# Kernel optimization log

Measured on AMD Instinct MI355X. Metric: run time of the kernel, lower is better.

Reference implementation:

```python
import jax, jax.numpy as jnp
import numpy as np

K_MASK = -2.3819763e+38
B, T, D, N, K, H = 2, 4096, 2048, 8, 1, 256


def apply_rope(inputs, positions, head_dim):
    # inputs: [B, T, n, H], positions: [B, T]
    fraction = 2.0 * jnp.arange(0, head_dim // 2, dtype=jnp.float32) / head_dim
    timescale = 10000.0 ** fraction  # [H/2]
    sinusoid_inp = positions[..., None].astype(jnp.float32) / timescale  # [B,T,H/2]
    sinusoid_inp = sinusoid_inp[..., None, :]  # [B,T,1,H/2]
    sin, cos = jnp.sin(sinusoid_inp), jnp.cos(sinusoid_inp)
    first_half, second_half = jnp.split(inputs, 2, axis=-1)
    first_part = first_half * cos - second_half * sin
    second_part = second_half * cos + first_half * sin
    return jnp.concatenate([first_part, second_part], axis=-1).astype(inputs.dtype)


def setup_inputs() -> dict:
    key = jax.random.key(0)
    kx, kq, kkv, ko = jax.random.split(key, 4)
    x = jax.random.normal(kx, (B, T, D), dtype=jnp.float32)
    segment_pos = jnp.broadcast_to(jnp.arange(T, dtype=jnp.int32), (B, T))
    attn_mask = jnp.broadcast_to(
        jnp.tril(jnp.ones((T, T), dtype=bool)), (B, T, T))  # causal
    q_w = jax.random.normal(kq, (N, D, H), dtype=jnp.float32) * 0.02
    kv_w = jax.random.normal(kkv, (2, K, D, H), dtype=jnp.float32) * 0.02
    out_w = jax.random.normal(ko, (N, H, D), dtype=jnp.float32) * 0.02
    return {"x": x, "segment_pos": segment_pos, "attn_mask": attn_mask,
            "q_w": q_w, "kv_w": kv_w, "out_w": out_w}


def reference(x, segment_pos, attn_mask, q_w, kv_w, out_w):
    # Projections (GQA branch: num_kv_heads != num_heads)
    query_proj = jnp.einsum('btd,ndh->btnh', x, q_w)          # [B,T,N,H]
    kv_proj = jnp.einsum('bsd,ckdh->cbskh', x, kv_w)          # [2,B,T,K,H]
    key_proj, value_proj = kv_proj[0], kv_proj[1]

    query_proj = apply_rope(query_proj, segment_pos, head_dim=H)
    query_scaled = query_proj * H ** (-0.5)
    key_proj = apply_rope(key_proj, segment_pos, head_dim=H)

    # Repeat KV heads for GQA (num_kv_heads == 1 -> N heads)
    value_proj = jnp.repeat(value_proj, N, axis=-2)           # [B,S,N,H]
    key_proj = jnp.repeat(key_proj, N, axis=-2)               # [B,S,N,H]

    logits = jnp.einsum('btnh,bsnh->btns', query_scaled, key_proj)
    padded_logits = jnp.where(attn_mask[:, :, None, :], logits, K_MASK)
    probs = jax.nn.softmax(padded_logits, axis=-1).astype(key_proj.dtype)
    encoded = jnp.einsum('btns,bsnh->btnh', probs, value_proj)
    attn_output = jnp.einsum('btnh,nhd->btd', encoded, out_w)
    return attn_output
```

## Files before the change

kernel.cpp:

```cpp
#include <hip/hip_runtime.h>

#define T_SEQ 4096
#define D_MODEL 2048
#define N_HEADS 8
#define HDIM 256

typedef unsigned int uint32;
typedef unsigned short u16;
typedef __attribute__((ext_vector_type(8))) short short8;
typedef __attribute__((ext_vector_type(4))) float f32x4;

__device__ __forceinline__ float bf2f(u16 v) {
  return __uint_as_float(((uint32)v) << 16);
}
__device__ __forceinline__ u16 f2bf(float f) {
  uint32 u = __float_as_uint(f);
  u += 0x7fffu + ((u >> 16) & 1u);
  return (u16)(u >> 16);
}
__device__ __forceinline__ uint2 pack4(const f32x4 v) {
  uint2 r;
  r.x = (uint32)f2bf(v[0]) | ((uint32)f2bf(v[1]) << 16);
  r.y = (uint32)f2bf(v[2]) | ((uint32)f2bf(v[3]) << 16);
  return r;
}
__device__ __forceinline__ void gload16(const u16* g, u16* l) {
  __builtin_amdgcn_global_load_lds(
      (const __attribute__((address_space(1))) unsigned int*)g,
      (__attribute__((address_space(3))) unsigned int*)l, 16, 0, 0);
}

__global__ __launch_bounds__(256) void convert_x(const float* __restrict__ x,
                                                 u16* __restrict__ xb) {
  const int idx = blockIdx.x * 256 + threadIdx.x;
  float4 v = *(const float4*)(x + (size_t)idx * 4);
  uint2 pk;
  pk.x = (uint32)f2bf(v.x) | ((uint32)f2bf(v.y) << 16);
  pk.y = (uint32)f2bf(v.z) | ((uint32)f2bf(v.w) << 16);
  *(uint2*)(xb + (size_t)idx * 4) = pk;
}

__global__ __launch_bounds__(256) void prep_weights(
    const float* __restrict__ qw, const float* __restrict__ kvw,
    const float* __restrict__ ow, u16* __restrict__ Wt, u16* __restrict__ Owt) {
  __shared__ float Ts[64][65];
  const int t = threadIdx.x;
  const int tx = blockIdx.x, ty = blockIdx.y, z = blockIdx.z;
  const float* src;
  int srcStride;
  u16* dst;
  if (z == 0) {
    const int c0 = tx * 64;
    const float* base = (c0 < 2048)
                            ? qw + (size_t)(c0 >> 8) * D_MODEL * HDIM
                            : kvw + (size_t)((c0 - 2048) >> 8) * D_MODEL * HDIM;
    src = base + (c0 & 255);
    srcStride = HDIM;
    dst = Wt + (size_t)c0 * D_MODEL;
  } else {
    if (tx >= 32) return;
    src = ow + tx * 64;
    srcStride = D_MODEL;
    dst = Owt + (size_t)tx * 64 * D_MODEL;
  }
  const int d0 = ty * 64;
  const int r = t >> 4, c4 = (t & 15) * 4;
#pragma unroll
  for (int i = 0; i < 4; ++i) {
    float4 v = *(const float4*)(src + (size_t)(d0 + r + i * 16) * srcStride + c4);
    *(float4*)&Ts[r + i * 16][c4] = v;
  }
  __syncthreads();
#pragma unroll
  for (int i = 0; i < 4; ++i) {
    const int crow = r + i * 16;
    uint2 pk;
    pk.x = (uint32)f2bf(Ts[c4 + 0][crow]) | ((uint32)f2bf(Ts[c4 + 1][crow]) << 16);
    pk.y = (uint32)f2bf(Ts[c4 + 2][crow]) | ((uint32)f2bf(Ts[c4 + 3][crow]) << 16);
    *(uint2*)(dst + (size_t)crow * D_MODEL + d0 + c4) = pk;
  }
}

__global__ __launch_bounds__(256) void gemm_qkv_mfma(
    const u16* __restrict__ xb, const u16* __restrict__ Wt,
    u16* __restrict__ Qb, u16* __restrict__ Kb, u16* __restrict__ Vt) {
  __shared__ u16 Asm[128][32];
  __shared__ u16 Bsm[128][32];
  const int t = threadIdx.x;
  const int w = t >> 6, l = t & 63, quad = l >> 4, lq = l & 15;
  const int wm = w & 1, wn = w >> 1;
  const int col0 = blockIdx.x * 128, row0 = blockIdx.y * 128;
  const u16* ga0 = xb + (size_t)(row0 + (t >> 2)) * D_MODEL + (t & 3) * 8;
  const u16* ga1 = ga0 + (size_t)64 * D_MODEL;
  const u16* gb0 = Wt + (size_t)(col0 + (t >> 2)) * D_MODEL + (t & 3) * 8;
  const u16* gb1 = gb0 + (size_t)64 * D_MODEL;
  u16* lA0 = &Asm[0][0] + t * 8;
  u16* lA1 = lA0 + 2048;
  u16* lB0 = &Bsm[0][0] + t * 8;
  u16* lB1 = lB0 + 2048;
  f32x4 acc[4][4];
#pragma unroll
  for (int i = 0; i < 4; ++i)
#pragma unroll
    for (int j = 0; j < 4; ++j) acc[i][j] = (f32x4){0.f, 0.f, 0.f, 0.f};
  for (int k0 = 0; k0 < D_MODEL; k0 += 32) {
    gload16(ga0 + k0, lA0);
    gload16(ga1 + k0, lA1);
    gload16(gb0 + k0, lB0);
    gload16(gb1 + k0, lB1);
    __syncthreads();
    short8 af[4], bf[4];
#pragma unroll
    for (int i = 0; i < 4; ++i)
      af[i] = *(const short8*)&Asm[wm * 64 + i * 16 + lq][quad * 8];
#pragma unroll
    for (int j = 0; j < 4; ++j)
      bf[j] = *(const short8*)&Bsm[wn * 64 + j * 16 + lq][quad * 8];
#pragma unroll
    for (int i = 0; i < 4; ++i)
#pragma unroll
      for (int j = 0; j < 4; ++j)
        acc[i][j] =
            __builtin_amdgcn_mfma_f32_16x16x32_bf16(af[i], bf[j], acc[i][j], 0, 0, 0);
    __syncthreads();
  }
  const int b = row0 >> 12, sbase = row0 & 4095;
#pragma unroll
  for (int i = 0; i < 4; ++i) {
    const int rowloc = wm * 64 + i * 16 + quad * 4;
#pragma unroll
    for (int j = 0; j < 4; ++j) {
      const int col = col0 + wn * 64 + j * 16 + lq;
      if (col < 2048) {
#pragma unroll
        for (int r = 0; r < 4; ++r)
          Qb[(size_t)(row0 + rowloc + r) * 2048 + col] = f2bf(acc[i][j][r]);
      } else if (col < 2304) {
#pragma unroll
        for (int r = 0; r < 4; ++r)
          Kb[(size_t)(row0 + rowloc + r) * HDIM + (col - 2048)] =
              f2bf(acc[i][j][r]);
      } else {
        *(uint2*)(Vt + ((size_t)b * HDIM + col - 2304) * T_SEQ + sbase + rowloc) =
            pack4(acc[i][j]);
      }
    }
  }
}

__global__ __launch_bounds__(256) void rope_kernel(u16* __restrict__ Qb,
                                                   u16* __restrict__ Kb,
                                                   const int* __restrict__ segpos) {
  const int bt = blockIdx.x;
  const int tid = threadIdx.x;
  const float fpos = (float)segpos[bt];
  const float k_ln = 9.210340371976184f / 128.0f;
  for (int p = tid; p < 1024; p += 256) {
    const int n = p >> 7, i = p & 127;
    const size_t base = (size_t)bt * (N_HEADS * HDIM) + (size_t)n * HDIM;
    const float th = fpos * expf(-(float)i * k_ln);
    float s, c;
    sincosf(th, &s, &c);
    const float f1 = bf2f(Qb[base + i]);
    const float f2 = bf2f(Qb[base + i + 128]);
    Qb[base + i] = f2bf((f1 * c - f2 * s) * 0.0625f);
    Qb[base + i + 128] = f2bf((f2 * c + f1 * s) * 0.0625f);
  }
  if (tid < 128) {
    const int i = tid;
    const size_t base = (size_t)bt * HDIM;
    const float th = fpos * expf(-(float)i * k_ln);
    float s, c;
    sincosf(th, &s, &c);
    const float f1 = bf2f(Kb[base + i]);
    const float f2 = bf2f(Kb[base + i + 128]);
    Kb[base + i] = f2bf(f1 * c - f2 * s);
    Kb[base + i + 128] = f2bf(f2 * c + f1 * s);
  }
}

__global__ __launch_bounds__(256) void attn_mfma(const u16* __restrict__ Qb,
                                                 const u16* __restrict__ Kb,
                                                 const u16* __restrict__ Vt,
                                                 u16* __restrict__ Eb) {
  __shared__ u16 Ks[32][264];
  __shared__ u16 Vs[256][40];
  __shared__ u16 Ps[4][16][40];
  const int t = threadIdx.x;
  const int w = t >> 6, l = t & 63;
  const int quad = l >> 4, lq = l & 15;
  const int bid = blockIdx.x;
  const int n = blockIdx.y, b = blockIdx.z;
  const u16* kgbase = Kb + (size_t)b * T_SEQ * HDIM;
  const u16* vgbase = Vt + (size_t)b * HDIM * T_SEQ;

#pragma unroll 1
  for (int ti = 0; ti < 2; ++ti) {
    const int qt = ti ? bid : 63 - bid;
    const int q0 = qt * 64;
    const int wrow0 = q0 + w * 16;

    short8 qf[8];
    {
      const u16* qbase = Qb +
          (((size_t)b * T_SEQ + wrow0 + lq) * N_HEADS + n) * HDIM + quad * 8;
#pragma unroll
      for (int c = 0; c < 8; ++c) qf[c] = *(const short8*)(qbase + c * 32);
    }
    f32x4 O[16];
#pragma unroll
    for (int i = 0; i < 16; ++i) O[i] = (f32x4){0.f, 0.f, 0.f, 0.f};
    float m_i[4] = {-1e30f, -1e30f, -1e30f, -1e30f};
    float l_i[4] = {0.f, 0.f, 0.f, 0.f};

    const int nst = 2 * qt + 2;
    for (int st = 0; st < nst; ++st) {
      const int s0 = st * 32;
      __syncthreads();
#pragma unroll
      for (int p = 0; p < 4; ++p) {
        const int chunk = p * 256 + t;
        const int row = chunk >> 5, col = chunk & 31;
        *(uint4*)&Ks[row][col * 8] =
            *(const uint4*)(kgbase + (size_t)(s0 + row) * HDIM + col * 8);
      }
#pragma unroll
      for (int p = 0; p < 4; ++p) {
        const int chunk = p * 256 + t;
        const int row = chunk >> 2, c4 = chunk & 3;
        *(uint4*)&Vs[row][c4 * 8] =
            *(const uint4*)(vgbase + (size_t)row * T_SEQ + s0 + c4 * 8);
      }
      __syncthreads();
      if (s0 <= wrow0 + 15) {
        f32x4 sa0 = (f32x4){0.f, 0.f, 0.f, 0.f};
        f32x4 sa1 = (f32x4){0.f, 0.f, 0.f, 0.f};
#pragma unroll
        for (int c = 0; c < 8; ++c) {
          short8 k0 = *(const short8*)&Ks[lq][c * 32 + quad * 8];
          short8 k1 = *(const short8*)&Ks[16 + lq][c * 32 + quad * 8];
          sa0 = __builtin_amdgcn_mfma_f32_16x16x32_bf16(qf[c], k0, sa0, 0, 0, 0);
          sa1 = __builtin_amdgcn_mfma_f32_16x16x32_bf16(qf[c], k1, sa1, 0, 0, 0);
        }
        if (s0 + 31 > wrow0) {
#pragma unroll
          for (int r = 0; r < 4; ++r) {
            const int rw = wrow0 + quad * 4 + r;
            if (s0 + lq > rw) sa0[r] = -1e30f;
            if (s0 + 16 + lq > rw) sa1[r] = -1e30f;
          }
        }
        float al[4];
#pragma unroll
        for (int r = 0; r < 4; ++r) {
          float mx = fmaxf(sa0[r], sa1[r]);
          mx = fmaxf(mx, __shfl_xor(mx, 1));
          mx = fmaxf(mx, __shfl_xor(mx, 2));
          mx = fmaxf(mx, __shfl_xor(mx, 4));
          mx = fmaxf(mx, __shfl_xor(mx, 8));
          const float mnew = fmaxf(m_i[r], mx);
          const float a = __expf(m_i[r] - mnew);
          const float p0 = __expf(sa0[r] - mnew);
          const float p1 = __expf(sa1[r] - mnew);
          float rs = p0 + p1;
          rs += __shfl_xor(rs, 1);
          rs += __shfl_xor(rs, 2);
          rs += __shfl_xor(rs, 4);
          rs += __shfl_xor(rs, 8);
          l_i[r] = l_i[r] * a + rs;
          m_i[r] = mnew;
          al[r] = a;
          Ps[w][quad * 4 + r][lq] = f2bf(p0);
          Ps[w][quad * 4 + r][16 + lq] = f2bf(p1);
        }
#pragma unroll
        for (int ntl = 0; ntl < 16; ++ntl) {
          O[ntl][0] *= al[0];
          O[ntl][1] *= al[1];
          O[ntl][2] *= al[2];
          O[ntl][3] *= al[3];
        }
        __asm__ volatile("s_waitcnt lgkmcnt(0)" ::: "memory");
        short8 pf = *(const short8*)&Ps[w][lq][quad * 8];
#pragma unroll
        for (int ntl = 0; ntl < 16; ++ntl) {
          short8 vf = *(const short8*)&Vs[ntl * 16 + lq][quad * 8];
          O[ntl] = __builtin_amdgcn_mfma_f32_16x16x32_bf16(pf, vf, O[ntl], 0, 0, 0);
        }
      }
    }
    float inv[4];
#pragma unroll
    for (int r = 0; r < 4; ++r) inv[r] = 1.0f / l_i[r];
    u16* ebase =
        Eb + (((size_t)b * T_SEQ + wrow0 + quad * 4) * N_HEADS + n) * HDIM + lq;
#pragma unroll
    for (int ntl = 0; ntl < 16; ++ntl)
#pragma unroll
      for (int r = 0; r < 4; ++r)
        ebase[(size_t)r * (N_HEADS * HDIM) + ntl * 16] = f2bf(O[ntl][r] * inv[r]);
  }
}

__global__ __launch_bounds__(256) void gemm_out_mfma(const u16* __restrict__ E,
                                                     const u16* __restrict__ Owt,
                                                     float* __restrict__ out) {
  __shared__ u16 Asm[128][32];
  __shared__ u16 Bsm[128][32];
  const int t = threadIdx.x;
  const int w = t >> 6, l = t & 63, quad = l >> 4, lq = l & 15;
  const int wm = w & 1, wn = w >> 1;
  const int col0 = blockIdx.x * 128, row0 = blockIdx.y * 128;
  const u16* ga0 = E + (size_t)(row0 + (t >> 2)) * D_MODEL + (t & 3) * 8;
  const u16* ga1 = ga0 + (size_t)64 * D_MODEL;
  const u16* gb0 = Owt + (size_t)(col0 + (t >> 2)) * D_MODEL + (t & 3) * 8;
  const u16* gb1 = gb0 + (size_t)64 * D_MODEL;
  u16* lA0 = &Asm[0][0] + t * 8;
  u16* lA1 = lA0 + 2048;
  u16* lB0 = &Bsm[0][0] + t * 8;
  u16* lB1 = lB0 + 2048;
  f32x4 acc[4][4];
#pragma unroll
  for (int i = 0; i < 4; ++i)
#pragma unroll
    for (int j = 0; j < 4; ++j) acc[i][j] = (f32x4){0.f, 0.f, 0.f, 0.f};
  for (int k0 = 0; k0 < D_MODEL; k0 += 32) {
    gload16(ga0 + k0, lA0);
    gload16(ga1 + k0, lA1);
    gload16(gb0 + k0, lB0);
    gload16(gb1 + k0, lB1);
    __syncthreads();
    short8 af[4], bf[4];
#pragma unroll
    for (int i = 0; i < 4; ++i)
      af[i] = *(const short8*)&Asm[wm * 64 + i * 16 + lq][quad * 8];
#pragma unroll
    for (int j = 0; j < 4; ++j)
      bf[j] = *(const short8*)&Bsm[wn * 64 + j * 16 + lq][quad * 8];
#pragma unroll
    for (int i = 0; i < 4; ++i)
#pragma unroll
      for (int j = 0; j < 4; ++j)
        acc[i][j] =
            __builtin_amdgcn_mfma_f32_16x16x32_bf16(af[i], bf[j], acc[i][j], 0, 0, 0);
    __syncthreads();
  }
#pragma unroll
  for (int i = 0; i < 4; ++i) {
    const int row = row0 + wm * 64 + i * 16 + quad * 4;
#pragma unroll
    for (int j = 0; j < 4; ++j) {
      const int col = col0 + wn * 64 + j * 16 + lq;
#pragma unroll
      for (int r = 0; r < 4; ++r)
        out[(size_t)(row + r) * D_MODEL + col] = acc[i][j][r];
    }
  }
}

extern "C" void kernel_launch(void* const* d_in, const int* in_sizes, int n_in,
                              void* d_out, int out_size, void* d_ws,
                              size_t ws_size, hipStream_t stream) {
  const float* x = (const float*)d_in[0];
  const int* segpos = (const int*)d_in[1];
  const float* qw = (const float*)d_in[3];
  const float* kvw = (const float*)d_in[4];
  const float* ow = (const float*)d_in[5];
  float* out = (float*)d_out;

  char* ws = (char*)d_ws;
  u16* Qb = (u16*)ws;
  u16* Kb = (u16*)(ws + (size_t)33554432);
  u16* Vt = (u16*)(ws + (size_t)37748736);
  u16* xb = (u16*)(ws + (size_t)41943040);
  u16* Eb = xb;
  u16* Wt = (u16*)(ws + (size_t)75497472);
  u16* Owt = (u16*)(ws + (size_t)85983232);

  hipLaunchKernelGGL(convert_x, dim3(16384), dim3(256), 0, stream, x, xb);
  hipLaunchKernelGGL(prep_weights, dim3(40, 32, 2), dim3(256), 0, stream, qw,
                     kvw, ow, Wt, Owt);
  hipLaunchKernelGGL(gemm_qkv_mfma, dim3(20, 64), dim3(256), 0, stream, xb, Wt,
                     Qb, Kb, Vt);
  hipLaunchKernelGGL(rope_kernel, dim3(8192), dim3(256), 0, stream, Qb, Kb,
                     segpos);
  hipLaunchKernelGGL(attn_mfma, dim3(32, N_HEADS, 2), dim3(256), 0, stream, Qb,
                     Kb, Vt, Eb);
  hipLaunchKernelGGL(gemm_out_mfma, dim3(16, 64), dim3(256), 0, stream, Eb, Owt,
                     out);
}
```

Measured before the change: 814.8 us.

## Read V fragments directly from global, defer row-sum reduction, skip unchanged rescale

Drops the shared-memory staging of V and loads each V fragment for the PV MFMA straight from global memory (relying on L2/L1 reuse across waves), which frees LDS and lets the launch bounds request three blocks per CU. The per-tile row-sum shuffle reduction is replaced by a per-lane partial sum, reduced once at the end. The O rescale is skipped when no row max increased in the wave. Ps padding is changed. The risk is higher global load latency and redundant V traffic in the inner loop, since each of the four waves now fetches the same V tile itself.

After: 1.156 ms. 1.42x slower.

```diff
diff --git a/kernel.cpp b/kernel.cpp
--- a/kernel.cpp
+++ b/kernel.cpp
@@ -179,13 +179,12 @@
   }
 }
 
-__global__ __launch_bounds__(256) void attn_mfma(const u16* __restrict__ Qb,
-                                                 const u16* __restrict__ Kb,
-                                                 const u16* __restrict__ Vt,
-                                                 u16* __restrict__ Eb) {
+__global__ __launch_bounds__(256, 3) void attn_mfma(const u16* __restrict__ Qb,
+                                                    const u16* __restrict__ Kb,
+                                                    const u16* __restrict__ Vt,
+                                                    u16* __restrict__ Eb) {
   __shared__ u16 Ks[32][264];
-  __shared__ u16 Vs[256][40];
-  __shared__ u16 Ps[4][16][40];
+  __shared__ u16 Ps[4][16][44];
   const int t = threadIdx.x;
   const int w = t >> 6, l = t & 63;
   const int quad = l >> 4, lq = l & 15;
@@ -211,7 +210,7 @@
 #pragma unroll
     for (int i = 0; i < 16; ++i) O[i] = (f32x4){0.f, 0.f, 0.f, 0.f};
     float m_i[4] = {-1e30f, -1e30f, -1e30f, -1e30f};
-    float l_i[4] = {0.f, 0.f, 0.f, 0.f};
+    float lsum[4] = {0.f, 0.f, 0.f, 0.f};
 
     const int nst = 2 * qt + 2;
     for (int st = 0; st < nst; ++st) {
@@ -224,13 +223,6 @@
         *(uint4*)&Ks[row][col * 8] =
             *(const uint4*)(kgbase + (size_t)(s0 + row) * HDIM + col * 8);
       }
-#pragma unroll
-      for (int p = 0; p < 4; ++p) {
-        const int chunk = p * 256 + t;
-        const int row = chunk >> 2, c4 = chunk & 3;
-        *(uint4*)&Vs[row][c4 * 8] =
-            *(const uint4*)(vgbase + (size_t)row * T_SEQ + s0 + c4 * 8);
-      }
       __syncthreads();
       if (s0 <= wrow0 + 15) {
         f32x4 sa0 = (f32x4){0.f, 0.f, 0.f, 0.f};
@@ -251,6 +243,7 @@
           }
         }
         float al[4];
+        int chg = 0;
 #pragma unroll
         for (int r = 0; r < 4; ++r) {
           float mx = fmaxf(sa0[r], sa1[r]);
@@ -258,40 +251,45 @@
           mx = fmaxf(mx, __shfl_xor(mx, 2));
           mx = fmaxf(mx, __shfl_xor(mx, 4));
           mx = fmaxf(mx, __shfl_xor(mx, 8));
+          if (mx > m_i[r]) chg = 1;
           const float mnew = fmaxf(m_i[r], mx);
-          const float a = __expf(m_i[r] - mnew);
+          al[r] = __expf(m_i[r] - mnew);
           const float p0 = __expf(sa0[r] - mnew);
           const float p1 = __expf(sa1[r] - mnew);
-          float rs = p0 + p1;
-          rs += __shfl_xor(rs, 1);
-          rs += __shfl_xor(rs, 2);
-          rs += __shfl_xor(rs, 4);
-          rs += __shfl_xor(rs, 8);
-          l_i[r] = l_i[r] * a + rs;
+          lsum[r] = fmaf(lsum[r], al[r], p0 + p1);
           m_i[r] = mnew;
-          al[r] = a;
           Ps[w][quad * 4 + r][lq] = f2bf(p0);
           Ps[w][quad * 4 + r][16 + lq] = f2bf(p1);
         }
-#pragma unroll
-        for (int ntl = 0; ntl < 16; ++ntl) {
-          O[ntl][0] *= al[0];
-          O[ntl][1] *= al[1];
-          O[ntl][2] *= al[2];
-          O[ntl][3] *= al[3];
+        if (__any(chg)) {
+#pragma unroll
+          for (int ntl = 0; ntl < 16; ++ntl) {
+            O[ntl][0] *= al[0];
+            O[ntl][1] *= al[1];
+            O[ntl][2] *= al[2];
+            O[ntl][3] *= al[3];
+          }
         }
         __asm__ volatile("s_waitcnt lgkmcnt(0)" ::: "memory");
         short8 pf = *(const short8*)&Ps[w][lq][quad * 8];
+        const u16* vrow = vgbase + (size_t)lq * T_SEQ + s0 + quad * 8;
 #pragma unroll
         for (int ntl = 0; ntl < 16; ++ntl) {
-          short8 vf = *(const short8*)&Vs[ntl * 16 + lq][quad * 8];
+          short8 vf = *(const short8*)(vrow + (size_t)(ntl * 16) * T_SEQ);
           O[ntl] = __builtin_amdgcn_mfma_f32_16x16x32_bf16(pf, vf, O[ntl], 0, 0, 0);
         }
       }
     }
     float inv[4];
 #pragma unroll
-    for (int r = 0; r < 4; ++r) inv[r] = 1.0f / l_i[r];
+    for (int r = 0; r < 4; ++r) {
+      float s = lsum[r];
+      s += __shfl_xor(s, 1);
+      s += __shfl_xor(s, 2);
+      s += __shfl_xor(s, 4);
+      s += __shfl_xor(s, 8);
+      inv[r] = 1.0f / s;
+    }
     u16* ebase =
         Eb + (((size_t)b * T_SEQ + wrow0 + quad * 4) * N_HEADS + n) * HDIM + lq;
 #pragma unroll
```
